# Kernel tuning notes

Measured on AMD Instinct MI355X. Metric: run time of the kernel, lower is better.

The kernel has to match this reference:

```python
import jax, jax.numpy as jnp
import numpy as np

N_NODES = 100000
N_EDGES = 1600000
FEAT = 64
HID = 64
N_LAYERS = 3
N_GRAPHS = 500


def setup_inputs() -> dict:
    key = jax.random.key(0)
    ks = jax.random.split(key, 8)
    x = jax.random.normal(ks[0], (N_NODES, FEAT), dtype=jnp.float32)
    edge_index = jax.random.randint(ks[1], (2, N_EDGES), 0, N_NODES, dtype=jnp.int64)
    mask = jax.random.randint(ks[2], (N_NODES,), 0, 2).astype(bool)
    batch = jnp.sort(jax.random.randint(ks[3], (N_NODES,), 0, N_GRAPHS, dtype=jnp.int64))
    Ws = jax.random.normal(ks[4], (N_LAYERS, HID, HID), dtype=jnp.float32) * 0.1
    bs = jnp.zeros((N_LAYERS, HID), dtype=jnp.float32)
    lt1_w = jax.random.normal(ks[5], (HID, 1), dtype=jnp.float32) * 0.1
    lt1_b = jnp.zeros((1,), dtype=jnp.float32)
    return {"x": x, "edge_index": edge_index, "mask": mask, "batch": batch,
            "Ws": Ws, "bs": bs, "lt1_w": lt1_w, "lt1_b": lt1_b}


def reference(x, edge_index, mask, batch, Ws, bs, lt1_w, lt1_b):
    n = x.shape[0]
    self_loop = jnp.arange(n, dtype=edge_index.dtype)
    src = jnp.concatenate([edge_index[0], self_loop])  # [E+N]
    dst = jnp.concatenate([edge_index[1], self_loop])
    # GCN symmetric normalization with self loops
    deg = jax.ops.segment_sum(jnp.ones_like(dst, dtype=x.dtype), dst, num_segments=n)
    dis = jax.lax.rsqrt(deg)  # deg >= 1 thanks to self loops
    norm = (dis[src] * dis[dst])[:, None]  # [E+N, 1]

    h = x
    for i in range(N_LAYERS):
        h = h @ Ws[i]                                   # [N, H] linear (no bias)
        msg = h[src] * norm                              # gather + scale
        h = jax.ops.segment_sum(msg, dst, num_segments=n) + bs[i]  # scatter-add + bias
        h = jax.nn.elu(h)
        # F.dropout with training=False is identity (eval mode)

    # global_mean_pool over masked nodes per graph
    m = mask.astype(h.dtype)
    num = jax.ops.segment_sum(h * m[:, None], batch, num_segments=N_GRAPHS)
    den = jax.ops.segment_sum(m, batch, num_segments=N_GRAPHS)
    pooled = num / jnp.maximum(den, 1.0)[:, None]        # [G, H]
    return pooled @ lt1_w + lt1_b                        # [G, 1]
```

## Files before the change

### kernel.cpp

```cpp
#include <hip/hip_runtime.h>
#include <math.h>

#define N_NODES 100000
#define N_EDGES 1600000
#define HID 64
#define N_LAYERS 3
#define N_GRAPHS 500

#define BUK_SHIFT 9
#define BUK_NODES 512
#define NBUK ((N_NODES + BUK_NODES - 1) / BUK_NODES)
#define BIN_BLOCKS 256
#define CHUNK ((N_EDGES + BIN_BLOCKS - 1) / BIN_BLOCKS)
#define BCAP 16384
#define PCAP 20480

typedef _Float16 half_t;
typedef __attribute__((ext_vector_type(8))) _Float16 f16x8;
typedef __attribute__((ext_vector_type(4))) float f32x4;
union H4 { ushort4 u; half_t h[4]; };

__device__ __forceinline__ float elu_f(float x) { return x > 0.f ? x : expm1f(x); }
__device__ __forceinline__ int pad8(int c) { return (c + 7) & ~7; }


__global__ void kA_bin(const int* __restrict__ ei, int* __restrict__ bcur,
                       unsigned int* __restrict__ bin) {
    __shared__ int h[NBUK];
    __shared__ int rsv[NBUK];
    for (int i = threadIdx.x; i < NBUK; i += 256) h[i] = 0;
    __syncthreads();
    int lo = blockIdx.x * CHUNK;
    int hi = min(lo + CHUNK, N_EDGES);
    for (int e = lo + (int)threadIdx.x; e < hi; e += 256)
        atomicAdd(&h[ei[N_EDGES + e] >> BUK_SHIFT], 1);
    __syncthreads();
    for (int i = threadIdx.x; i < NBUK; i += 256) {
        int c = h[i];
        rsv[i] = c ? atomicAdd(&bcur[i], c) : 0;
        h[i] = 0;
    }
    __syncthreads();
    for (int e = lo + (int)threadIdx.x; e < hi; e += 256) {
        int d = ei[N_EDGES + e];
        int s = ei[e];
        int b = d >> BUK_SHIFT;
        int pos = rsv[b] + atomicAdd(&h[b], 1);
        if (pos < BCAP)
            bin[(size_t)b * BCAP + pos] = (unsigned)s | ((unsigned)(d & (BUK_NODES - 1)) << 17);
    }
}

__global__ void kB_build(const unsigned int* __restrict__ bin,
                         const int* __restrict__ bcur,
                         int* __restrict__ poff, int* __restrict__ plen,
                         float* __restrict__ dis, int* __restrict__ psrc,
                         half_t* __restrict__ B16) {
    __shared__ int cnt[BUK_NODES];
    __shared__ int excl[BUK_NODES];
    __shared__ int ps[256];
    int b = blockIdx.x;
    int t = threadIdx.x;
    int ecnt = min(bcur[b], BCAP);
    size_t e0 = (size_t)b * BCAP;
    size_t p0 = (size_t)b * PCAP;
    int n0 = b << BUK_SHIFT;

    if (b == 0 && t < HID) B16[(size_t)N_NODES * HID + t] = (half_t)0.f;

    cnt[t] = 0; cnt[t + 256] = 0;
    __syncthreads();
    for (int e = t; e < ecnt; e += 256)
        atomicAdd(&cnt[bin[e0 + e] >> 17], 1);
    __syncthreads();
    int pc0 = pad8(cnt[2 * t]), pc1 = pad8(cnt[2 * t + 1]);
    int psum = pc0 + pc1;
    ps[t] = psum;
    __syncthreads();
    for (int o = 1; o < 256; o <<= 1) {
        int u = (t >= o) ? ps[t - o] : 0;
        __syncthreads();
        ps[t] += u;
        __syncthreads();
    }
    int pexcl = ps[t] - psum;
    excl[2 * t] = pexcl;
    excl[2 * t + 1] = pexcl + pc0;
    int ptot = ps[255];
    __syncthreads();
    for (int i = t; i < BUK_NODES; i += 256) {
        int n = n0 + i;
        if (n < N_NODES) {
            poff[n] = (int)p0 + excl[i];
            plen[n] = pad8(cnt[i]);
            dis[n] = rsqrtf((float)cnt[i] + 1.0f);
        }
    }
    for (int j = t; j < ptot; j += 256) psrc[p0 + j] = N_NODES;
    __syncthreads();
    cnt[t] = excl[t]; cnt[t + 256] = excl[t + 256];
    __syncthreads();
    for (int e = t; e < ecnt; e += 256) {
        unsigned v = bin[e0 + e];
        int dloc = v >> 17;
        int pos = atomicAdd(&cnt[dloc], 1);
        if (pos < PCAP) psrc[p0 + pos] = (int)(v & 0x1FFFFu);
    }
}

__global__ void k_w16t(const float* __restrict__ Ws, half_t* __restrict__ W16T) {
    int i = blockIdx.x * 256 + threadIdx.x;
    if (i >= N_LAYERS * HID * HID) return;
    int l = i >> 12;
    int k = (i >> 6) & 63;
    int c = i & 63;
    W16T[(size_t)l * 4096 + c * 64 + k] = (half_t)Ws[(size_t)l * 4096 + k * 64 + c];
}

__device__ __forceinline__ f16x8 make_afrag(const float* Xf, const half_t* Xh,
                                            const float* bias, int act,
                                            size_t rowbase, int k) {
    f16x8 a;
    if (act) {
        f16x8 xu = *(const f16x8*)(Xh + rowbase + k);
        float4 ba = *(const float4*)(bias + k);
        float4 bb = *(const float4*)(bias + k + 4);
        a[0] = (half_t)elu_f((float)xu[0] + ba.x);
        a[1] = (half_t)elu_f((float)xu[1] + ba.y);
        a[2] = (half_t)elu_f((float)xu[2] + ba.z);
        a[3] = (half_t)elu_f((float)xu[3] + ba.w);
        a[4] = (half_t)elu_f((float)xu[4] + bb.x);
        a[5] = (half_t)elu_f((float)xu[5] + bb.y);
        a[6] = (half_t)elu_f((float)xu[6] + bb.z);
        a[7] = (half_t)elu_f((float)xu[7] + bb.w);
    } else {
        float4 xa = *(const float4*)(Xf + rowbase + k);
        float4 xb = *(const float4*)(Xf + rowbase + k + 4);
        a[0] = (half_t)xa.x; a[1] = (half_t)xa.y;
        a[2] = (half_t)xa.z; a[3] = (half_t)xa.w;
        a[4] = (half_t)xb.x; a[5] = (half_t)xb.y;
        a[6] = (half_t)xb.z; a[7] = (half_t)xb.w;
    }
    return a;
}

__global__ void k_gemm(const float* __restrict__ Xf, const half_t* __restrict__ Xh,
                       const half_t* __restrict__ wt, const float* __restrict__ bias,
                       int act, const float* __restrict__ dis,
                       half_t* __restrict__ B16, int n) {
    int lane = threadIdx.x & 63;
    int wid = (blockIdx.x * blockDim.x + threadIdx.x) >> 6;
    int r0 = wid << 4;
    if (r0 >= n) return;
    size_t rowbase = (size_t)(r0 + (lane & 15)) * HID;
    int goff = (lane >> 4) * 8;

    f16x8 a0 = make_afrag(Xf, Xh, bias, act, rowbase, goff);
    f16x8 a1 = make_afrag(Xf, Xh, bias, act, rowbase, 32 + goff);

    int wcol = (lane & 15) * HID + goff;
    f32x4 c0 = {0.f, 0.f, 0.f, 0.f}, c1 = c0, c2 = c0, c3 = c0;
    {
        f16x8 b0 = *(const f16x8*)&wt[wcol];
        f16x8 b1 = *(const f16x8*)&wt[wcol + 32];
        c0 = __builtin_amdgcn_mfma_f32_16x16x32_f16(a0, b0, c0, 0, 0, 0);
        c0 = __builtin_amdgcn_mfma_f32_16x16x32_f16(a1, b1, c0, 0, 0, 0);
    }
    {
        f16x8 b0 = *(const f16x8*)&wt[1024 + wcol];
        f16x8 b1 = *(const f16x8*)&wt[1024 + wcol + 32];
        c1 = __builtin_amdgcn_mfma_f32_16x16x32_f16(a0, b0, c1, 0, 0, 0);
        c1 = __builtin_amdgcn_mfma_f32_16x16x32_f16(a1, b1, c1, 0, 0, 0);
    }
    {
        f16x8 b0 = *(const f16x8*)&wt[2048 + wcol];
        f16x8 b1 = *(const f16x8*)&wt[2048 + wcol + 32];
        c2 = __builtin_amdgcn_mfma_f32_16x16x32_f16(a0, b0, c2, 0, 0, 0);
        c2 = __builtin_amdgcn_mfma_f32_16x16x32_f16(a1, b1, c2, 0, 0, 0);
    }
    {
        f16x8 b0 = *(const f16x8*)&wt[3072 + wcol];
        f16x8 b1 = *(const f16x8*)&wt[3072 + wcol + 32];
        c3 = __builtin_amdgcn_mfma_f32_16x16x32_f16(a0, b0, c3, 0, 0, 0);
        c3 = __builtin_amdgcn_mfma_f32_16x16x32_f16(a1, b1, c3, 0, 0, 0);
    }

    int rg = (lane >> 4) * 4;
    int col = lane & 15;
#pragma unroll
    for (int r = 0; r < 4; r++) {
        int row = r0 + rg + r;
        float dv = dis[row];
        size_t rb = (size_t)row * HID;
        B16[rb + col]      = (half_t)(c0[r] * dv);
        B16[rb + 16 + col] = (half_t)(c1[r] * dv);
        B16[rb + 32 + col] = (half_t)(c2[r] * dv);
        B16[rb + 48 + col] = (half_t)(c3[r] * dv);
    }
}

__global__ void k_agg(const int* __restrict__ poff, const int* __restrict__ plen,
                      const int* __restrict__ psrc,
                      const float* __restrict__ dis, const half_t* __restrict__ B16,
                      half_t* __restrict__ A16, int n) {
    int lane = threadIdx.x & 63;
    int node = __builtin_amdgcn_readfirstlane((blockIdx.x * blockDim.x + threadIdx.x) >> 6);
    if (node >= n) return;
    float acc = (float)B16[(size_t)node * HID + lane];
    int p = poff[node];
    int p1 = p + plen[node];
    for (; p + 16 <= p1; p += 16) {
        int s[16];
#pragma unroll
        for (int i = 0; i < 16; i++) s[i] = psrc[p + i];
        float v[16];
#pragma unroll
        for (int i = 0; i < 16; i++) v[i] = (float)B16[(size_t)s[i] * HID + lane];
        acc += (((v[0] + v[1]) + (v[2] + v[3])) + ((v[4] + v[5]) + (v[6] + v[7])))
             + (((v[8] + v[9]) + (v[10] + v[11])) + ((v[12] + v[13]) + (v[14] + v[15])));
    }
    if (p < p1) {
        int s[8];
#pragma unroll
        for (int i = 0; i < 8; i++) s[i] = psrc[p + i];
        float v[8];
#pragma unroll
        for (int i = 0; i < 8; i++) v[i] = (float)B16[(size_t)s[i] * HID + lane];
        acc += ((v[0] + v[1]) + (v[2] + v[3])) + ((v[4] + v[5]) + (v[6] + v[7]));
    }
    A16[(size_t)node * HID + lane] = (half_t)(acc * dis[node]);
}

__global__ void k_pool_final(const half_t* __restrict__ A16, const float* __restrict__ bias,
                             const int* __restrict__ mask, const int* __restrict__ batch,
                             const float* __restrict__ w, const float* __restrict__ b,
                             float* __restrict__ out) {
    __shared__ float sacc[4][HID];
    __shared__ float scnt[4];
    int g = blockIdx.x;
    int t = threadIdx.x;
    int lane = t & 63;
    int wv = t >> 6;

    int lo = 0, hi = N_NODES;
    while (lo < hi) { int mid = (lo + hi) >> 1; if (batch[mid] < g) lo = mid + 1; else hi = mid; }
    int n0 = lo;
    hi = N_NODES;
    while (lo < hi) { int mid = (lo + hi) >> 1; if (batch[mid] < g + 1) lo = mid + 1; else hi = mid; }
    int n1 = lo;

    float bl = bias[lane];
    float acc0 = 0.f, acc1 = 0.f;
    float cnt0 = 0.f, cnt1 = 0.f;
    int n = n0 + wv;
    for (; n + 4 < n1; n += 8) {
        int m0 = mask[n], m1 = mask[n + 4];
        float v0 = (float)A16[(size_t)n * HID + lane];
        float v1 = (float)A16[(size_t)(n + 4) * HID + lane];
        if (m0) { acc0 += elu_f(v0 + bl); cnt0 += 1.f; }
        if (m1) { acc1 += elu_f(v1 + bl); cnt1 += 1.f; }
    }
    if (n < n1 && mask[n]) { acc0 += elu_f((float)A16[(size_t)n * HID + lane] + bl); cnt0 += 1.f; }
    acc0 += acc1; cnt0 += cnt1;

    sacc[wv][lane] = acc0;
    if (lane == 0) scnt[wv] = cnt0;
    __syncthreads();
    if (wv == 0) {
        float v = sacc[0][lane] + sacc[1][lane] + sacc[2][lane] + sacc[3][lane];
        float c = scnt[0] + scnt[1] + scnt[2] + scnt[3];
        v = v / fmaxf(c, 1.0f) * w[lane];
#pragma unroll
        for (int o = 32; o > 0; o >>= 1) v += __shfl_down(v, o);
        if (lane == 0) out[g] = v + b[0];
    }
}

extern "C" void kernel_launch(void* const* d_in, const int* in_sizes, int n_in,
                              void* d_out, int out_size, void* d_ws, size_t ws_size,
                              hipStream_t stream) {
    const float* x     = (const float*)d_in[0];
    const int*   ei    = (const int*)d_in[1];
    const int*   mask  = (const int*)d_in[2];
    const int*   batch = (const int*)d_in[3];
    const float* Ws    = (const float*)d_in[4];
    const float* bs    = (const float*)d_in[5];
    const float* lw    = (const float*)d_in[6];
    const float* lb    = (const float*)d_in[7];
    float* out = (float*)d_out;

    half_t* A16  = (half_t*)d_ws;
    half_t* B16  = A16 + (size_t)N_NODES * HID;
    float*  dis  = (float*)(B16 + (size_t)(N_NODES + 1) * HID);
    int*    poff = (int*)(dis + N_NODES);
    int*    plen = poff + N_NODES;
    int*    bcur = plen + N_NODES;
    half_t* W16T = (half_t*)(bcur + 200);
    int*    psrc = (int*)(W16T + (size_t)N_LAYERS * HID * HID);
    unsigned int* bin = (unsigned int*)(psrc + (size_t)NBUK * PCAP);

    hipMemsetAsync(bcur, 0, NBUK * sizeof(int), stream);

    kA_bin<<<BIN_BLOCKS, 256, 0, stream>>>(ei, bcur, bin);
    kB_build<<<NBUK, 256, 0, stream>>>(bin, bcur, poff, plen, dis, psrc, B16);
    k_w16t<<<(N_LAYERS * HID * HID + 255) / 256, 256, 0, stream>>>(Ws, W16T);

    const int gemm_blocks = (N_NODES / 16 + 3) / 4;
    const int row_blocks  = (N_NODES + 3) / 4;
    for (int l = 0; l < N_LAYERS; l++) {
        const float* bias_in = (l == 0) ? bs : bs + (l - 1) * HID;
        k_gemm<<<gemm_blocks, 256, 0, stream>>>((l == 0) ? x : nullptr,
                                                (l == 0) ? nullptr : A16,
                                                W16T + (size_t)l * HID * HID,
                                                bias_in, (l == 0) ? 0 : 1,
                                                dis, B16, N_NODES);
        k_agg<<<row_blocks, 256, 0, stream>>>(poff, plen, psrc, dis, B16, A16, N_NODES);
    }

    k_pool_final<<<N_GRAPHS, 256, 0, stream>>>(A16, bs + 2 * HID, mask, batch, lw, lb, out);
}
```

Measured before the change: 234.4 us.

## Fuse aggregation with next layer's GEMM and fold weight transpose into build

Aggregation for layers 1 and 2 now runs in a combined kernel. Each wave gathers 16 nodes sequentially, applies bias and ELU, stages the rows in LDS, and runs the MFMA for the next layer into a ping-pong B buffer. This removes the A16 round trip and two launches. The weight transpose kernel is folded into kB_build. The cost is that each wave now processes 16 nodes one after another, so there is far less gather parallelism per wave (6250 waves instead of 100k). That could hurt latency hiding in the memory-bound gather.

New measurement: 237.9 us. No clear change (+1.5%).

```diff
diff --git a/kernel.cpp b/kernel.cpp
--- a/kernel.cpp
+++ b/kernel.cpp
@@ -18,7 +18,6 @@
 typedef _Float16 half_t;
 typedef __attribute__((ext_vector_type(8))) _Float16 f16x8;
 typedef __attribute__((ext_vector_type(4))) float f32x4;
-union H4 { ushort4 u; half_t h[4]; };
 
 __device__ __forceinline__ float elu_f(float x) { return x > 0.f ? x : expm1f(x); }
 __device__ __forceinline__ int pad8(int c) { return (c + 7) & ~7; }
@@ -55,7 +54,8 @@
                          const int* __restrict__ bcur,
                          int* __restrict__ poff, int* __restrict__ plen,
                          float* __restrict__ dis, int* __restrict__ psrc,
-                         half_t* __restrict__ B16) {
+                         half_t* __restrict__ Ba, half_t* __restrict__ Bb,
+                         const float* __restrict__ Ws, half_t* __restrict__ W16T) {
     __shared__ int cnt[BUK_NODES];
     __shared__ int excl[BUK_NODES];
     __shared__ int ps[256];
@@ -66,7 +66,15 @@
     size_t p0 = (size_t)b * PCAP;
     int n0 = b << BUK_SHIFT;
 
-    if (b == 0 && t < HID) B16[(size_t)N_NODES * HID + t] = (half_t)0.f;
+    if (b == 0 && t < HID) {
+        Ba[(size_t)N_NODES * HID + t] = (half_t)0.f;
+        Bb[(size_t)N_NODES * HID + t] = (half_t)0.f;
+    }
+    if (b < 48) {
+        int i = b * 256 + t;
+        int l = i >> 12, k = (i >> 6) & 63, c = i & 63;
+        W16T[(size_t)l * 4096 + c * 64 + k] = (half_t)Ws[(size_t)l * 4096 + k * 64 + c];
+    }
 
     cnt[t] = 0; cnt[t + 256] = 0;
     __syncthreads();
@@ -108,56 +116,37 @@
     }
 }
 
-__global__ void k_w16t(const float* __restrict__ Ws, half_t* __restrict__ W16T) {
-    int i = blockIdx.x * 256 + threadIdx.x;
-    if (i >= N_LAYERS * HID * HID) return;
-    int l = i >> 12;
-    int k = (i >> 6) & 63;
-    int c = i & 63;
-    W16T[(size_t)l * 4096 + c * 64 + k] = (half_t)Ws[(size_t)l * 4096 + k * 64 + c];
-}
-
-__device__ __forceinline__ f16x8 make_afrag(const float* Xf, const half_t* Xh,
-                                            const float* bias, int act,
-                                            size_t rowbase, int k) {
-    f16x8 a;
-    if (act) {
-        f16x8 xu = *(const f16x8*)(Xh + rowbase + k);
-        float4 ba = *(const float4*)(bias + k);
-        float4 bb = *(const float4*)(bias + k + 4);
-        a[0] = (half_t)elu_f((float)xu[0] + ba.x);
-        a[1] = (half_t)elu_f((float)xu[1] + ba.y);
-        a[2] = (half_t)elu_f((float)xu[2] + ba.z);
-        a[3] = (half_t)elu_f((float)xu[3] + ba.w);
-        a[4] = (half_t)elu_f((float)xu[4] + bb.x);
-        a[5] = (half_t)elu_f((float)xu[5] + bb.y);
-        a[6] = (half_t)elu_f((float)xu[6] + bb.z);
-        a[7] = (half_t)elu_f((float)xu[7] + bb.w);
-    } else {
-        float4 xa = *(const float4*)(Xf + rowbase + k);
-        float4 xb = *(const float4*)(Xf + rowbase + k + 4);
-        a[0] = (half_t)xa.x; a[1] = (half_t)xa.y;
-        a[2] = (half_t)xa.z; a[3] = (half_t)xa.w;
-        a[4] = (half_t)xb.x; a[5] = (half_t)xb.y;
-        a[6] = (half_t)xb.z; a[7] = (half_t)xb.w;
-    }
-    return a;
-}
-
-__global__ void k_gemm(const float* __restrict__ Xf, const half_t* __restrict__ Xh,
-                       const half_t* __restrict__ wt, const float* __restrict__ bias,
-                       int act, const float* __restrict__ dis,
-                       half_t* __restrict__ B16, int n) {
-    int lane = threadIdx.x & 63;
-    int wid = (blockIdx.x * blockDim.x + threadIdx.x) >> 6;
-    int r0 = wid << 4;
-    if (r0 >= n) return;
-    size_t rowbase = (size_t)(r0 + (lane & 15)) * HID;
+
+__device__ __forceinline__ float gather_row(const int* __restrict__ psrc,
+                                            const half_t* __restrict__ B,
+                                            int p, int p1, int lane, float acc) {
+    for (; p + 16 <= p1; p += 16) {
+        int s[16];
+#pragma unroll
+        for (int i = 0; i < 16; i++) s[i] = psrc[p + i];
+        float v[16];
+#pragma unroll
+        for (int i = 0; i < 16; i++) v[i] = (float)B[(size_t)s[i] * HID + lane];
+        acc += (((v[0] + v[1]) + (v[2] + v[3])) + ((v[4] + v[5]) + (v[6] + v[7])))
+             + (((v[8] + v[9]) + (v[10] + v[11])) + ((v[12] + v[13]) + (v[14] + v[15])));
+    }
+    if (p < p1) {
+        int s[8];
+#pragma unroll
+        for (int i = 0; i < 8; i++) s[i] = psrc[p + i];
+        float v[8];
+#pragma unroll
+        for (int i = 0; i < 8; i++) v[i] = (float)B[(size_t)s[i] * HID + lane];
+        acc += ((v[0] + v[1]) + (v[2] + v[3])) + ((v[4] + v[5]) + (v[6] + v[7]));
+    }
+    return acc;
+}
+
+__device__ __forceinline__ void mfma_rows(f16x8 a0, f16x8 a1,
+                                          const half_t* __restrict__ wt, int lane,
+                                          const float* __restrict__ dis, int r0,
+                                          half_t* __restrict__ Bout) {
     int goff = (lane >> 4) * 8;
-
-    f16x8 a0 = make_afrag(Xf, Xh, bias, act, rowbase, goff);
-    f16x8 a1 = make_afrag(Xf, Xh, bias, act, rowbase, 32 + goff);
-
     int wcol = (lane & 15) * HID + goff;
     f32x4 c0 = {0.f, 0.f, 0.f, 0.f}, c1 = c0, c2 = c0, c3 = c0;
     {
@@ -184,7 +173,6 @@
         c3 = __builtin_amdgcn_mfma_f32_16x16x32_f16(a0, b0, c3, 0, 0, 0);
         c3 = __builtin_amdgcn_mfma_f32_16x16x32_f16(a1, b1, c3, 0, 0, 0);
     }
-
     int rg = (lane >> 4) * 4;
     int col = lane & 15;
 #pragma unroll
@@ -192,42 +180,70 @@
         int row = r0 + rg + r;
         float dv = dis[row];
         size_t rb = (size_t)row * HID;
-        B16[rb + col]      = (half_t)(c0[r] * dv);
-        B16[rb + 16 + col] = (half_t)(c1[r] * dv);
-        B16[rb + 32 + col] = (half_t)(c2[r] * dv);
-        B16[rb + 48 + col] = (half_t)(c3[r] * dv);
-    }
+        Bout[rb + col]      = (half_t)(c0[r] * dv);
+        Bout[rb + 16 + col] = (half_t)(c1[r] * dv);
+        Bout[rb + 32 + col] = (half_t)(c2[r] * dv);
+        Bout[rb + 48 + col] = (half_t)(c3[r] * dv);
+    }
+}
+
+
+__global__ void k_gemm0(const float* __restrict__ X, const half_t* __restrict__ wt,
+                        const float* __restrict__ dis, half_t* __restrict__ Bout, int n) {
+    int lane = threadIdx.x & 63;
+    int wid = (blockIdx.x * blockDim.x + threadIdx.x) >> 6;
+    int r0 = wid << 4;
+    if (r0 >= n) return;
+    size_t rowbase = (size_t)(r0 + (lane & 15)) * HID;
+    int goff = (lane >> 4) * 8;
+    f16x8 a0, a1;
+#pragma unroll
+    for (int j = 0; j < 8; j++) a0[j] = (half_t)X[rowbase + goff + j];
+#pragma unroll
+    for (int j = 0; j < 8; j++) a1[j] = (half_t)X[rowbase + 32 + goff + j];
+    mfma_rows(a0, a1, wt, lane, dis, r0, Bout);
+}
+
+__global__ void k_agg_gemm(const int* __restrict__ poff, const int* __restrict__ plen,
+                           const int* __restrict__ psrc, const float* __restrict__ dis,
+                           const half_t* __restrict__ Bin, const half_t* __restrict__ wt,
+                           const float* __restrict__ bias,
+                           half_t* __restrict__ Bout, int n) {
+    __shared__ half_t tile[4][16 * 72];
+    int lane = threadIdx.x & 63;
+    int wv = threadIdx.x >> 6;
+    int wid = (blockIdx.x * blockDim.x + threadIdx.x) >> 6;
+    int r0 = wid << 4;
+    if (r0 >= n) return;
+    half_t* tl = tile[wv];
+    float bl = bias[lane];
+
+    for (int j = 0; j < 16; j++) {
+        int node = r0 + j;
+        float acc = (float)Bin[(size_t)node * HID + lane];
+        int p = poff[node];
+        acc = gather_row(psrc, Bin, p, p + plen[node], lane, acc);
+        tl[j * 72 + lane] = (half_t)elu_f(acc * dis[node] + bl);
+    }
+    asm volatile("s_waitcnt lgkmcnt(0)" ::: "memory");
+    __builtin_amdgcn_sched_barrier(0);
+
+    int goff = (lane >> 4) * 8;
+    f16x8 a0 = *(const f16x8*)&tl[(lane & 15) * 72 + goff];
+    f16x8 a1 = *(const f16x8*)&tl[(lane & 15) * 72 + 32 + goff];
+    mfma_rows(a0, a1, wt, lane, dis, r0, Bout);
 }
 
 __global__ void k_agg(const int* __restrict__ poff, const int* __restrict__ plen,
                       const int* __restrict__ psrc,
-                      const float* __restrict__ dis, const half_t* __restrict__ B16,
+                      const float* __restrict__ dis, const half_t* __restrict__ Bin,
                       half_t* __restrict__ A16, int n) {
     int lane = threadIdx.x & 63;
     int node = __builtin_amdgcn_readfirstlane((blockIdx.x * blockDim.x + threadIdx.x) >> 6);
     if (node >= n) return;
-    float acc = (float)B16[(size_t)node * HID + lane];
+    float acc = (float)Bin[(size_t)node * HID + lane];
     int p = poff[node];
-    int p1 = p + plen[node];
-    for (; p + 16 <= p1; p += 16) {
-        int s[16];
-#pragma unroll
-        for (int i = 0; i < 16; i++) s[i] = psrc[p + i];
-        float v[16];
-#pragma unroll
-        for (int i = 0; i < 16; i++) v[i] = (float)B16[(size_t)s[i] * HID + lane];
-        acc += (((v[0] + v[1]) + (v[2] + v[3])) + ((v[4] + v[5]) + (v[6] + v[7])))
-             + (((v[8] + v[9]) + (v[10] + v[11])) + ((v[12] + v[13]) + (v[14] + v[15])));
-    }
-    if (p < p1) {
-        int s[8];
-#pragma unroll
-        for (int i = 0; i < 8; i++) s[i] = psrc[p + i];
-        float v[8];
-#pragma unroll
-        for (int i = 0; i < 8; i++) v[i] = (float)B16[(size_t)s[i] * HID + lane];
-        acc += ((v[0] + v[1]) + (v[2] + v[3])) + ((v[4] + v[5]) + (v[6] + v[7]));
-    }
+    acc = gather_row(psrc, Bin, p, p + plen[node], lane, acc);
     A16[(size_t)node * HID + lane] = (half_t)(acc * dis[node]);
 }
 
@@ -290,8 +306,9 @@
     float* out = (float*)d_out;
 
     half_t* A16  = (half_t*)d_ws;
-    half_t* B16  = A16 + (size_t)N_NODES * HID;
-    float*  dis  = (float*)(B16 + (size_t)(N_NODES + 1) * HID);
+    half_t* Ba   = A16 + (size_t)N_NODES * HID;
+    half_t* Bb   = Ba + (size_t)(N_NODES + 1) * HID;
+    float*  dis  = (float*)(Bb + (size_t)(N_NODES + 1) * HID);
     int*    poff = (int*)(dis + N_NODES);
     int*    plen = poff + N_NODES;
     int*    bcur = plen + N_NODES;
@@ -302,20 +319,18 @@
     hipMemsetAsync(bcur, 0, NBUK * sizeof(int), stream);
 
     kA_bin<<<BIN_BLOCKS, 256, 0, stream>>>(ei, bcur, bin);
-    kB_build<<<NBUK, 256, 0, stream>>>(bin, bcur, poff, plen, dis, psrc, B16);
-    k_w16t<<<(N_LAYERS * HID * HID + 255) / 256, 256, 0, stream>>>(Ws, W16T);
-
-    const int gemm_blocks = (N_NODES / 16 + 3) / 4;
+    kB_build<<<NBUK, 256, 0, stream>>>(bin, bcur, poff, plen, dis, psrc,
+                                       Ba, Bb, Ws, W16T);
+
+    const int wave_blocks = (N_NODES / 16 + 3) / 4;
     const int row_blocks  = (N_NODES + 3) / 4;
-    for (int l = 0; l < N_LAYERS; l++) {
-        const float* bias_in = (l == 0) ? bs : bs + (l - 1) * HID;
-        k_gemm<<<gemm_blocks, 256, 0, stream>>>((l == 0) ? x : nullptr,
-                                                (l == 0) ? nullptr : A16,
-                                                W16T + (size_t)l * HID * HID,
-                                                bias_in, (l == 0) ? 0 : 1,
-                                                dis, B16, N_NODES);
-        k_agg<<<row_blocks, 256, 0, stream>>>(poff, plen, psrc, dis, B16, A16, N_NODES);
-    }
+
+    k_gemm0<<<wave_blocks, 256, 0, stream>>>(x, W16T, dis, Ba, N_NODES);
+    k_agg_gemm<<<wave_blocks, 256, 0, stream>>>(poff, plen, psrc, dis, Ba,
+                                                W16T + 4096, bs, Bb, N_NODES);
+    k_agg_gemm<<<wave_blocks, 256, 0, stream>>>(poff, plen, psrc, dis, Bb,
+                                                W16T + 8192, bs + HID, Ba, N_NODES);
+    k_agg<<<row_blocks, 256, 0, stream>>>(poff, plen, psrc, dis, Ba, A16, N_NODES);
 
     k_pool_final<<<N_GRAPHS, 256, 0, stream>>>(A16, bs + 2 * HID, mask, batch, lw, lb, out);
 }
```
